# Kernel optimization log

Hardware: AMD Instinct MI355X
Metric: run time of the kernel (lower is better)

The kernel has to match this reference:

```python
import jax, jax.numpy as jnp
import numpy as np

B, N, C = 16, 65536, 21          # batch, anchors, classes (class 0 = background)
TH_CONF = 0.05                   # confidence threshold
TH_IOU = 0.5                     # NMS IoU threshold
TOP_K = 200                      # candidates kept per (batch, class) before NMS
V0, V1 = 0.1, 0.2                # SSD box-coder variances


def setup_inputs() -> dict:
    key = jax.random.key(0)
    k1, k2, k3, k4 = jax.random.split(key, 4)
    conf = jax.random.normal(k1, (B, N, C), dtype=jnp.float32)
    loc = jax.random.normal(k2, (B, N, 4), dtype=jnp.float32)
    # anchors in center form (cx, cy, w, h), normalized coords
    cxcy = jax.random.uniform(k3, (N, 2), dtype=jnp.float32)
    wh = 0.02 + 0.2 * jax.random.uniform(k4, (N, 2), dtype=jnp.float32)
    anchors = jnp.concatenate([cxcy, wh], axis=-1)
    return {"conf": conf, "loc": loc, "anchors": anchors}


def _decode(anchors, loc):
    # SSD decode: anchors [N,4] center form, loc [B,N,4] offsets -> [B,N,4] xyxy
    a_xy, a_wh = anchors[:, :2], anchors[:, 2:]
    xy = a_xy + loc[..., :2] * V0 * a_wh
    wh = a_wh * jnp.exp(loc[..., 2:] * V1)
    return jnp.concatenate([xy - 0.5 * wh, xy + 0.5 * wh], axis=-1)


def _iou(boxes):
    # boxes [K,4] xyxy -> pairwise IoU [K,K]
    area = jnp.maximum(boxes[:, 2] - boxes[:, 0], 0.0) * jnp.maximum(boxes[:, 3] - boxes[:, 1], 0.0)
    lt = jnp.maximum(boxes[:, None, :2], boxes[None, :, :2])
    rb = jnp.minimum(boxes[:, None, 2:], boxes[None, :, 2:])
    wh = jnp.maximum(rb - lt, 0.0)
    inter = wh[..., 0] * wh[..., 1]
    union = area[:, None] + area[None, :] - inter
    return inter / jnp.maximum(union, 1e-9)


def _nms_keep(iou, valid):
    # greedy NMS over score-sorted candidates; valid = (score >= TH_CONF)
    K = iou.shape[0]
    idx = jnp.arange(K)

    def body(keep, xs):
        row, v, i = xs
        suppressed = jnp.any((row > TH_IOU) & keep & (idx < i))
        k = v & (~suppressed)
        return keep.at[i].set(k), 0

    keep, _ = jax.lax.scan(body, jnp.zeros((K,), dtype=bool), (iou, valid, idx))
    return keep


def reference(conf, loc, anchors):
    score = jax.nn.softmax(conf, axis=2)            # [B,N,C]
    boxes = _decode(anchors, loc)                   # [B,N,4]
    # skip background class 0 (cls_base = 1 for softmax classifier)
    cls_scores = jnp.swapaxes(score[..., 1:], 1, 2)  # [B,C-1,N]
    top_s, top_i = jax.lax.top_k(cls_scores, TOP_K)  # [B,C-1,K], sorted desc
    top_boxes = jax.vmap(lambda bx, ix: bx[ix])(boxes, top_i)  # [B,C-1,K,4]
    valid = top_s >= TH_CONF
    keep = jax.vmap(jax.vmap(lambda b, v: _nms_keep(_iou(b), v)))(top_boxes, valid)  # [B,C-1,K]
    out_boxes = jnp.where(keep[..., None], top_boxes, 0.0)
    out_scores = jnp.where(keep, top_s, 0.0)
    return jnp.concatenate([out_boxes, out_scores[..., None]], axis=-1)  # [B,C-1,K,5]
```

## Files before the change

### kernel.cpp

```cpp
#include <hip/hip_runtime.h>
#include <stdint.h>

#define NB     16
#define NANCH  65536
#define NC     21
#define NCLS   20
#define NCOL   (NB * NCLS)
#define TOPK   200
#define NBINS  2048
#define CAP    256
#define CAPCOL 4096

constexpr float TH      = 0.05f;
constexpr float TPRE    = 0.15f;
constexpr float SCALE15 = (float)NBINS / 0.85f;
constexpr float SCALE05 = (float)NBINS / 0.95f;

__device__ __forceinline__ int bin15(float s) {
  int b = (int)((s - 0.15f) * SCALE15);
  return b < 0 ? 0 : (b > NBINS - 1 ? NBINS - 1 : b);
}
__device__ __forceinline__ int bin05(float s) {
  int b = (int)((s - 0.05f) * SCALE05);
  return b < 0 ? 0 : (b > NBINS - 1 ? NBINS - 1 : b);
}

__device__ __forceinline__ void softmax_row(const float* __restrict__ conf,
                                            long long a, float* e, float& S) {
  const float* row = conf + a * NC;
  float x[NC];
#pragma unroll
  for (int c = 0; c < NC; ++c) x[c] = row[c];
  float m = x[0];
#pragma unroll
  for (int c = 1; c < NC; ++c) m = fmaxf(m, x[c]);
#pragma unroll
  for (int c = 0; c < NC; ++c) e[c] = expf(x[c] - m);
  float r0 = e[0] + e[8],  r1 = e[1] + e[9],  r2 = e[2] + e[10], r3 = e[3] + e[11];
  float r4 = e[4] + e[12], r5 = e[5] + e[13], r6 = e[6] + e[14], r7 = e[7] + e[15];
  S = ((r0 + r1) + (r2 + r3)) + ((r4 + r5) + (r6 + r7));
  S += e[16]; S += e[17]; S += e[18]; S += e[19]; S += e[20];
}

__global__ __launch_bounds__(256) void softmax_collect_kernel(
    const float* __restrict__ conf,
    unsigned int* __restrict__ cnt, unsigned long long* __restrict__ cand) {
  const int tid = threadIdx.x;
  const int a = blockIdx.x * 256 + tid;
  const int b = a >> 16;
  const int n = a & (NANCH - 1);
  float e[NC], S;
  softmax_row(conf, (long long)a, e, S);
  float sc[NCLS];
  unsigned int takemask = 0;
#pragma unroll
  for (int c = 0; c < NCLS; ++c) {
    sc[c] = e[c + 1] / S;
    if (sc[c] >= TPRE) takemask |= (1u << c);
  }

  __shared__ unsigned int wcnt[4][NCLS];
  __shared__ unsigned int wbase[4][NCLS];
  const int wave = tid >> 6, lane = tid & 63;
#pragma unroll
  for (int c = 0; c < NCLS; ++c) {
    unsigned long long m = __ballot((takemask >> c) & 1);
    if (lane == 0) wcnt[wave][c] = (unsigned int)__popcll(m);
  }
  __syncthreads();
  if (tid < NCLS) {
    const int c = tid;
    unsigned int t0 = wcnt[0][c], t1 = wcnt[1][c], t2 = wcnt[2][c], t3 = wcnt[3][c];
    unsigned int tot = t0 + t1 + t2 + t3;
    unsigned int base = tot ? atomicAdd(&cnt[b * NCLS + c], tot) : 0u;
    wbase[0][c] = base;
    wbase[1][c] = base + t0;
    wbase[2][c] = base + t0 + t1;
    wbase[3][c] = base + t0 + t1 + t2;
  }
  __syncthreads();
#pragma unroll
  for (int c = 0; c < NCLS; ++c) {
    bool take = (takemask >> c) & 1;
    unsigned long long m = __ballot(take);
    if (take) {
      unsigned int off = wbase[wave][c] +
                         (unsigned int)__popcll(m & ((1ULL << lane) - 1));
      if (off < CAPCOL) {
        unsigned int key = __float_as_uint(sc[c]) | 0x80000000u;
        cand[(long long)(b * NCLS + c) * CAPCOL + off] =
            ((unsigned long long)(key ^ 0xFFFFFFFFu) << 32) |
            (unsigned long long)(unsigned int)n;
      }
    }
  }
}

__device__ __forceinline__ int find_sel(unsigned int* hist, unsigned int* part,
                                        unsigned int* suf, int* s_sel, int tid) {
  unsigned int p = 0;
#pragma unroll
  for (int i = 0; i < NBINS / 256; ++i) p += hist[tid * (NBINS / 256) + i];
  part[tid] = p;
  __syncthreads();
  if (tid == 0) {
    unsigned int run = 0;
    for (int t = 255; t >= 0; --t) { suf[t] = run; run += part[t]; }
    *s_sel = -1;
  }
  __syncthreads();
  unsigned int above = suf[tid];
  if (above < TOPK && above + part[tid] >= TOPK) {
    unsigned int cum = above; int sb = tid * (NBINS / 256);
    for (int i = NBINS / 256 - 1; i >= 0; --i) {
      unsigned int c = hist[tid * (NBINS / 256) + i];
      if (cum + c >= TOPK) { sb = tid * (NBINS / 256) + i; break; }
      cum += c;
    }
    *s_sel = sb;
  }
  __syncthreads();
  return *s_sel;
}

__global__ __launch_bounds__(256) void topk_nms_kernel(
    const unsigned long long* __restrict__ candg,
    const unsigned int* __restrict__ cnt,
    const float* __restrict__ conf, const float* __restrict__ loc,
    const float* __restrict__ anchors, float* __restrict__ out) {
  const int bc = blockIdx.x;
  const int b  = bc / NCLS;
  const int cls = bc % NCLS;
  const int tid = threadIdx.x;

  __shared__ unsigned int hist[NBINS];
  __shared__ unsigned int part[256], suf[256];
  __shared__ int s_sel, s_n;
  __shared__ unsigned long long cand[CAP];
  __shared__ float bx[TOPK][4];
  __shared__ float barea[TOPK];
  __shared__ float bscore[TOPK];
  __shared__ unsigned long long adj[TOPK][4];
  __shared__ unsigned char keepf[TOPK];

  int nc = (int)cnt[bc];
  const bool fast = (nc >= TOPK && nc <= CAPCOL);
  for (int i = tid; i < NBINS; i += 256) hist[i] = 0;
  if (tid == 0) s_n = 0;
  __syncthreads();

  const unsigned long long* cg = candg + (long long)bc * CAPCOL;
  if (fast) {
    for (int i = tid; i < nc; i += 256) {
      unsigned int key = (unsigned int)(cg[i] >> 32) ^ 0xFFFFFFFFu;
      float s = __uint_as_float(key ^ 0x80000000u);
      atomicAdd(&hist[bin15(s)], 1u);
    }
    __syncthreads();
    int sel = find_sel(hist, part, suf, &s_sel, tid);
    for (int i = tid; i < nc; i += 256) {
      unsigned long long k64 = cg[i];
      unsigned int key = (unsigned int)(k64 >> 32) ^ 0xFFFFFFFFu;
      float s = __uint_as_float(key ^ 0x80000000u);
      if (bin15(s) >= sel) {
        int pos = atomicAdd(&s_n, 1);
        if (pos < CAP) cand[pos] = k64;
      }
    }
  } else {
    for (int n = tid; n < NANCH; n += 256) {
      float e[NC], S;
      softmax_row(conf, (long long)b * NANCH + n, e, S);
      float s = e[cls + 1] / S;
      if (s >= TH) atomicAdd(&hist[bin05(s)], 1u);
    }
    __syncthreads();
    int sel = find_sel(hist, part, suf, &s_sel, tid);
    for (int n = tid; n < NANCH; n += 256) {
      float e[NC], S;
      softmax_row(conf, (long long)b * NANCH + n, e, S);
      float s = e[cls + 1] / S;
      if (s >= TH && (sel < 0 || bin05(s) >= sel)) {
        int pos = atomicAdd(&s_n, 1);
        if (pos < CAP) {
          unsigned int key = __float_as_uint(s) | 0x80000000u;
          cand[pos] = ((unsigned long long)(key ^ 0xFFFFFFFFu) << 32) |
                      (unsigned long long)(unsigned int)n;
        }
      }
    }
  }
  __syncthreads();
  int ncand = s_n; if (ncand > CAP) ncand = CAP;
  for (int i = tid; i < CAP; i += 256) if (i >= ncand) cand[i] = ~0ULL;
  __syncthreads();

  for (int k = 2; k <= CAP; k <<= 1) {
    for (int j = k >> 1; j > 0; j >>= 1) {
      int partner = tid ^ j;
      unsigned long long mine = cand[tid];
      unsigned long long theirs = cand[partner];
      bool dirUp = ((tid & k) == 0);
      bool keepMin = (tid < partner) == dirUp;
      unsigned long long v = ((mine < theirs) == keepMin) ? mine : theirs;
      __syncthreads();
      cand[tid] = v;
      __syncthreads();
    }
  }
  const int nsel = (ncand < TOPK) ? ncand : TOPK;

  if (tid < TOPK) {
    if (tid < nsel) {
      unsigned long long sk = cand[tid];
      unsigned int key = (unsigned int)(sk >> 32) ^ 0xFFFFFFFFu;
      float s = __uint_as_float(key ^ 0x80000000u);
      int idx = (int)(unsigned int)(sk & 0xFFFFFFFFu);
      float4 anc = ((const float4*)anchors)[idx];
      float4 l   = ((const float4*)loc)[(long long)b * NANCH + idx];
      float cx = anc.x + (l.x * 0.1f) * anc.z;
      float cy = anc.y + (l.y * 0.1f) * anc.w;
      float w  = anc.z * expf(l.z * 0.2f);
      float h  = anc.w * expf(l.w * 0.2f);
      float x1 = cx - 0.5f * w, y1 = cy - 0.5f * h;
      float x2 = cx + 0.5f * w, y2 = cy + 0.5f * h;
      bx[tid][0] = x1; bx[tid][1] = y1; bx[tid][2] = x2; bx[tid][3] = y2;
      barea[tid] = fmaxf(x2 - x1, 0.0f) * fmaxf(y2 - y1, 0.0f);
      bscore[tid] = s;
    } else {
      bx[tid][0] = bx[tid][1] = bx[tid][2] = bx[tid][3] = 0.0f;
      barea[tid] = 0.0f; bscore[tid] = 0.0f;
    }
  }
  __syncthreads();

  if (tid < TOPK) {
    float ax1 = bx[tid][0], ay1 = bx[tid][1], ax2 = bx[tid][2], ay2 = bx[tid][3];
    float aar = barea[tid];
    for (int w = 0; w < 4; ++w) {
      unsigned long long mword = 0;
      int lim = (w < 3) ? 64 : (TOPK - 192);
      for (int jj = 0; jj < lim; ++jj) {
        int j = (w << 6) + jj;
        float ltx = fmaxf(ax1, bx[j][0]);
        float lty = fmaxf(ay1, bx[j][1]);
        float rbx = fminf(ax2, bx[j][2]);
        float rby = fminf(ay2, bx[j][3]);
        float iw = fmaxf(rbx - ltx, 0.0f);
        float ih = fmaxf(rby - lty, 0.0f);
        float inter = iw * ih;
        float uni = aar + barea[j] - inter;
        float iou = inter / fmaxf(uni, 1e-9f);
        if (iou > 0.5f) mword |= (1ULL << jj);
      }
      adj[tid][w] = mword;
    }
  }
  __syncthreads();

  if (tid == 0) {
    unsigned long long s0 = 0, s1 = 0, s2 = 0, s3 = 0;
    for (int i = 0; i < 64; ++i) {
      bool kept = (i < nsel) && !((s0 >> i) & 1ULL);
      keepf[i] = kept ? 1 : 0;
      if (kept) { s0 |= adj[i][0]; s1 |= adj[i][1]; s2 |= adj[i][2]; s3 |= adj[i][3]; }
    }
    for (int i = 64; i < 128; ++i) {
      bool kept = (i < nsel) && !((s1 >> (i - 64)) & 1ULL);
      keepf[i] = kept ? 1 : 0;
      if (kept) { s0 |= adj[i][0]; s1 |= adj[i][1]; s2 |= adj[i][2]; s3 |= adj[i][3]; }
    }
    for (int i = 128; i < 192; ++i) {
      bool kept = (i < nsel) && !((s2 >> (i - 128)) & 1ULL);
      keepf[i] = kept ? 1 : 0;
      if (kept) { s0 |= adj[i][0]; s1 |= adj[i][1]; s2 |= adj[i][2]; s3 |= adj[i][3]; }
    }
    for (int i = 192; i < TOPK; ++i) {
      bool kept = (i < nsel) && !((s3 >> (i - 192)) & 1ULL);
      keepf[i] = kept ? 1 : 0;
      if (kept) { s0 |= adj[i][0]; s1 |= adj[i][1]; s2 |= adj[i][2]; s3 |= adj[i][3]; }
    }
  }
  __syncthreads();

  if (tid < TOPK) {
    float* o = out + ((long long)bc * TOPK + tid) * 5;
    bool k = keepf[tid] != 0;
    o[0] = k ? bx[tid][0] : 0.0f;
    o[1] = k ? bx[tid][1] : 0.0f;
    o[2] = k ? bx[tid][2] : 0.0f;
    o[3] = k ? bx[tid][3] : 0.0f;
    o[4] = k ? bscore[tid] : 0.0f;
  }
}

extern "C" void kernel_launch(void* const* d_in, const int* in_sizes, int n_in,
                              void* d_out, int out_size, void* d_ws, size_t ws_size,
                              hipStream_t stream) {
  const float* conf    = (const float*)d_in[0];
  const float* loc     = (const float*)d_in[1];
  const float* anchors = (const float*)d_in[2];
  float* out = (float*)d_out;

  char* ws = (char*)d_ws;
  unsigned long long* cand = (unsigned long long*)ws;
  unsigned int*       cnt  = (unsigned int*)(ws + 10485760);

  hipMemsetAsync(ws + 10485760, 0, 1280, stream);
  softmax_collect_kernel<<<(NB * NANCH) / 256, 256, 0, stream>>>(conf, cnt, cand);
  topk_nms_kernel<<<NCOL, 256, 0, stream>>>(cand, cnt, conf, loc, anchors, out);
}
```

Measured before the change: 110.7 us.

## Stage conf through LDS, cache candidates, shuffle-based sort and parallel scan

```diff
diff --git a/kernel.cpp b/kernel.cpp
--- a/kernel.cpp
+++ b/kernel.cpp
@@ -25,12 +25,14 @@
   return b < 0 ? 0 : (b > NBINS - 1 ? NBINS - 1 : b);
 }
 
-__device__ __forceinline__ void softmax_row(const float* __restrict__ conf,
-                                            long long a, float* e, float& S) {
-  const float* row = conf + a * NC;
-  float x[NC];
-#pragma unroll
-  for (int c = 0; c < NC; ++c) x[c] = row[c];
+__device__ __forceinline__ unsigned long long shflx64(unsigned long long v, int m) {
+  unsigned int lo = (unsigned int)v, hi = (unsigned int)(v >> 32);
+  lo = __shfl_xor(lo, m);
+  hi = __shfl_xor(hi, m);
+  return ((unsigned long long)hi << 32) | lo;
+}
+
+__device__ __forceinline__ void softmax_tail(const float* x, float* e, float& S) {
   float m = x[0];
 #pragma unroll
   for (int c = 1; c < NC; ++c) m = fmaxf(m, x[c]);
@@ -46,11 +48,22 @@
     const float* __restrict__ conf,
     unsigned int* __restrict__ cnt, unsigned long long* __restrict__ cand) {
   const int tid = threadIdx.x;
+  __shared__ float ld[256 * NC];
+  const float4* src = (const float4*)conf + (long long)blockIdx.x * 1344;
+  float4* dst4 = (float4*)ld;
+#pragma unroll
+  for (int i = 0; i < 5; ++i) dst4[tid + i * 256] = src[tid + i * 256];
+  if (tid < 64) dst4[tid + 1280] = src[tid + 1280];
+  __syncthreads();
+
   const int a = blockIdx.x * 256 + tid;
   const int b = a >> 16;
   const int n = a & (NANCH - 1);
+  float x[NC];
+#pragma unroll
+  for (int c = 0; c < NC; ++c) x[c] = ld[tid * NC + c];
   float e[NC], S;
-  softmax_row(conf, (long long)a, e, S);
+  softmax_tail(x, e, S);
   float sc[NCLS];
   unsigned int takemask = 0;
 #pragma unroll
@@ -97,27 +110,37 @@
 }
 
 __device__ __forceinline__ int find_sel(unsigned int* hist, unsigned int* part,
-                                        unsigned int* suf, int* s_sel, int tid) {
+                                        int* s_sel, int tid) {
   unsigned int p = 0;
 #pragma unroll
-  for (int i = 0; i < NBINS / 256; ++i) p += hist[tid * (NBINS / 256) + i];
+  for (int i = 0; i < 8; ++i) p += hist[tid * 8 + i];
   part[tid] = p;
-  __syncthreads();
-  if (tid == 0) {
-    unsigned int run = 0;
-    for (int t = 255; t >= 0; --t) { suf[t] = run; run += part[t]; }
-    *s_sel = -1;
-  }
-  __syncthreads();
-  unsigned int above = suf[tid];
-  if (above < TOPK && above + part[tid] >= TOPK) {
-    unsigned int cum = above; int sb = tid * (NBINS / 256);
-    for (int i = NBINS / 256 - 1; i >= 0; --i) {
-      unsigned int c = hist[tid * (NBINS / 256) + i];
-      if (cum + c >= TOPK) { sb = tid * (NBINS / 256) + i; break; }
-      cum += c;
-    }
-    *s_sel = sb;
+  if (tid == 0) *s_sel = -1;
+  __syncthreads();
+  if (tid < 64) {
+    unsigned int p4 = part[tid * 4] + part[tid * 4 + 1] +
+                      part[tid * 4 + 2] + part[tid * 4 + 3];
+    unsigned int sfx = p4;
+#pragma unroll
+    for (int off = 1; off < 64; off <<= 1) {
+      unsigned int o = __shfl_down(sfx, off);
+      if (tid + off < 64) sfx += o;
+    }
+    unsigned int above = sfx - p4;
+    if (above < TOPK && sfx >= TOPK) {
+      unsigned int cum = above; int sel = tid * 32; bool found = false;
+      for (int q = 3; q >= 0 && !found; --q) {
+        unsigned int pc = part[tid * 4 + q];
+        if (cum + pc >= TOPK) {
+          for (int i = 7; i >= 0; --i) {
+            unsigned int c = hist[(tid * 4 + q) * 8 + i];
+            if (cum + c >= TOPK) { sel = (tid * 4 + q) * 8 + i; found = true; break; }
+            cum += c;
+          }
+        } else cum += pc;
+      }
+      *s_sel = sel;
+    }
   }
   __syncthreads();
   return *s_sel;
@@ -133,13 +156,13 @@
   const int cls = bc % NCLS;
   const int tid = threadIdx.x;
 
+  __shared__ unsigned long long cg_lds[CAPCOL];
   __shared__ unsigned int hist[NBINS];
-  __shared__ unsigned int part[256], suf[256];
+  __shared__ unsigned int part[256];
   __shared__ int s_sel, s_n;
   __shared__ unsigned long long cand[CAP];
-  __shared__ float bx[TOPK][4];
+  __shared__ float bx[TOPK][5];
   __shared__ float barea[TOPK];
-  __shared__ float bscore[TOPK];
   __shared__ unsigned long long adj[TOPK][4];
   __shared__ unsigned char keepf[TOPK];
 
@@ -149,17 +172,19 @@
   if (tid == 0) s_n = 0;
   __syncthreads();
 
-  const unsigned long long* cg = candg + (long long)bc * CAPCOL;
   if (fast) {
+    const unsigned long long* cg = candg + (long long)bc * CAPCOL;
     for (int i = tid; i < nc; i += 256) {
-      unsigned int key = (unsigned int)(cg[i] >> 32) ^ 0xFFFFFFFFu;
+      unsigned long long k64 = cg[i];
+      cg_lds[i] = k64;
+      unsigned int key = (unsigned int)(k64 >> 32) ^ 0xFFFFFFFFu;
       float s = __uint_as_float(key ^ 0x80000000u);
       atomicAdd(&hist[bin15(s)], 1u);
     }
     __syncthreads();
-    int sel = find_sel(hist, part, suf, &s_sel, tid);
+    int sel = find_sel(hist, part, &s_sel, tid);
     for (int i = tid; i < nc; i += 256) {
-      unsigned long long k64 = cg[i];
+      unsigned long long k64 = cg_lds[i];
       unsigned int key = (unsigned int)(k64 >> 32) ^ 0xFFFFFFFFu;
       float s = __uint_as_float(key ^ 0x80000000u);
       if (bin15(s) >= sel) {
@@ -169,16 +194,22 @@
     }
   } else {
     for (int n = tid; n < NANCH; n += 256) {
-      float e[NC], S;
-      softmax_row(conf, (long long)b * NANCH + n, e, S);
+      const float* row = conf + ((long long)b * NANCH + n) * NC;
+      float x[NC], e[NC], S;
+#pragma unroll
+      for (int c = 0; c < NC; ++c) x[c] = row[c];
+      softmax_tail(x, e, S);
       float s = e[cls + 1] / S;
       if (s >= TH) atomicAdd(&hist[bin05(s)], 1u);
     }
     __syncthreads();
-    int sel = find_sel(hist, part, suf, &s_sel, tid);
+    int sel = find_sel(hist, part, &s_sel, tid);
     for (int n = tid; n < NANCH; n += 256) {
-      float e[NC], S;
-      softmax_row(conf, (long long)b * NANCH + n, e, S);
+      const float* row = conf + ((long long)b * NANCH + n) * NC;
+      float x[NC], e[NC], S;
+#pragma unroll
+      for (int c = 0; c < NC; ++c) x[c] = row[c];
+      softmax_tail(x, e, S);
       float s = e[cls + 1] / S;
       if (s >= TH && (sel < 0 || bin05(s) >= sel)) {
         int pos = atomicAdd(&s_n, 1);
@@ -192,30 +223,31 @@
   }
   __syncthreads();
   int ncand = s_n; if (ncand > CAP) ncand = CAP;
-  for (int i = tid; i < CAP; i += 256) if (i >= ncand) cand[i] = ~0ULL;
-  __syncthreads();
-
+
+  unsigned long long v = (tid < ncand) ? cand[tid] : ~0ULL;
   for (int k = 2; k <= CAP; k <<= 1) {
-    for (int j = k >> 1; j > 0; j >>= 1) {
-      int partner = tid ^ j;
-      unsigned long long mine = cand[tid];
-      unsigned long long theirs = cand[partner];
-      bool dirUp = ((tid & k) == 0);
-      bool keepMin = (tid < partner) == dirUp;
-      unsigned long long v = ((mine < theirs) == keepMin) ? mine : theirs;
-      __syncthreads();
+    const bool up = ((tid & k) == 0);
+    for (int j = k >> 1; j >= 64; j >>= 1) {
       cand[tid] = v;
       __syncthreads();
+      unsigned long long o = cand[tid ^ j];
+      bool keepMin = (((tid & j) == 0) == up);
+      v = ((v < o) == keepMin) ? v : o;
+      __syncthreads();
+    }
+    for (int j = (k >> 1) < 32 ? (k >> 1) : 32; j >= 1; j >>= 1) {
+      unsigned long long o = shflx64(v, j);
+      bool keepMin = (((tid & j) == 0) == up);
+      v = ((v < o) == keepMin) ? v : o;
     }
   }
   const int nsel = (ncand < TOPK) ? ncand : TOPK;
 
   if (tid < TOPK) {
     if (tid < nsel) {
-      unsigned long long sk = cand[tid];
-      unsigned int key = (unsigned int)(sk >> 32) ^ 0xFFFFFFFFu;
+      unsigned int key = (unsigned int)(v >> 32) ^ 0xFFFFFFFFu;
       float s = __uint_as_float(key ^ 0x80000000u);
-      int idx = (int)(unsigned int)(sk & 0xFFFFFFFFu);
+      int idx = (int)(unsigned int)(v & 0xFFFFFFFFu);
       float4 anc = ((const float4*)anchors)[idx];
       float4 l   = ((const float4*)loc)[(long long)b * NANCH + idx];
       float cx = anc.x + (l.x * 0.1f) * anc.z;
@@ -225,11 +257,11 @@
       float x1 = cx - 0.5f * w, y1 = cy - 0.5f * h;
       float x2 = cx + 0.5f * w, y2 = cy + 0.5f * h;
       bx[tid][0] = x1; bx[tid][1] = y1; bx[tid][2] = x2; bx[tid][3] = y2;
+      bx[tid][4] = s;
       barea[tid] = fmaxf(x2 - x1, 0.0f) * fmaxf(y2 - y1, 0.0f);
-      bscore[tid] = s;
     } else {
-      bx[tid][0] = bx[tid][1] = bx[tid][2] = bx[tid][3] = 0.0f;
-      barea[tid] = 0.0f; bscore[tid] = 0.0f;
+      bx[tid][0] = bx[tid][1] = bx[tid][2] = bx[tid][3] = bx[tid][4] = 0.0f;
+      barea[tid] = 0.0f;
     }
   }
   __syncthreads();
@@ -261,24 +293,32 @@
   if (tid == 0) {
     unsigned long long s0 = 0, s1 = 0, s2 = 0, s3 = 0;
     for (int i = 0; i < 64; ++i) {
+      unsigned long long m0 = adj[i][0], m1 = adj[i][1],
+                         m2 = adj[i][2], m3 = adj[i][3];
       bool kept = (i < nsel) && !((s0 >> i) & 1ULL);
       keepf[i] = kept ? 1 : 0;
-      if (kept) { s0 |= adj[i][0]; s1 |= adj[i][1]; s2 |= adj[i][2]; s3 |= adj[i][3]; }
+      if (kept) { s0 |= m0; s1 |= m1; s2 |= m2; s3 |= m3; }
     }
     for (int i = 64; i < 128; ++i) {
+      unsigned long long m0 = adj[i][0], m1 = adj[i][1],
+                         m2 = adj[i][2], m3 = adj[i][3];
       bool kept = (i < nsel) && !((s1 >> (i - 64)) & 1ULL);
       keepf[i] = kept ? 1 : 0;
-      if (kept) { s0 |= adj[i][0]; s1 |= adj[i][1]; s2 |= adj[i][2]; s3 |= adj[i][3]; }
+      if (kept) { s0 |= m0; s1 |= m1; s2 |= m2; s3 |= m3; }
     }
     for (int i = 128; i < 192; ++i) {
+      unsigned long long m0 = adj[i][0], m1 = adj[i][1],
+                         m2 = adj[i][2], m3 = adj[i][3];
       bool kept = (i < nsel) && !((s2 >> (i - 128)) & 1ULL);
       keepf[i] = kept ? 1 : 0;
-      if (kept) { s0 |= adj[i][0]; s1 |= adj[i][1]; s2 |= adj[i][2]; s3 |= adj[i][3]; }
+      if (kept) { s0 |= m0; s1 |= m1; s2 |= m2; s3 |= m3; }
     }
     for (int i = 192; i < TOPK; ++i) {
+      unsigned long long m0 = adj[i][0], m1 = adj[i][1],
+                         m2 = adj[i][2], m3 = adj[i][3];
       bool kept = (i < nsel) && !((s3 >> (i - 192)) & 1ULL);
       keepf[i] = kept ? 1 : 0;
-      if (kept) { s0 |= adj[i][0]; s1 |= adj[i][1]; s2 |= adj[i][2]; s3 |= adj[i][3]; }
+      if (kept) { s0 |= m0; s1 |= m1; s2 |= m2; s3 |= m3; }
     }
   }
   __syncthreads();
@@ -290,7 +330,7 @@
     o[1] = k ? bx[tid][1] : 0.0f;
     o[2] = k ? bx[tid][2] : 0.0f;
     o[3] = k ? bx[tid][3] : 0.0f;
-    o[4] = k ? bscore[tid] : 0.0f;
+    o[4] = k ? bx[tid][4] : 0.0f;
   }
 }
 
```

Result: no change. 108.6 us (-1.9%).
